# Kernel tuning notes

Hardware: AMD Instinct MI355X
Metric: run time of the kernel (lower is better)

Reference implementation:

```python
import jax, jax.numpy as jnp
import numpy as np

DIM = 256
N_PATCHES = 2048
N_HEADS = 8
BATCH = 2


def setup_inputs() -> dict:
    key = jax.random.key(0)
    ks = jax.random.split(key, 8)
    d = DIM
    s = d ** -0.5
    return {
        "x": jax.random.normal(ks[0], (BATCH, N_PATCHES, d), dtype=jnp.float32),
        # weights stored (in_features, out_features) so y = x @ W + b
        "W_qk": jax.random.normal(ks[1], (d, 2 * d), dtype=jnp.float32) * s,
        "W_v": jax.random.normal(ks[2], (d, d), dtype=jnp.float32) * s,
        "W_proj": jax.random.normal(ks[3], (d, d), dtype=jnp.float32) * s,
        "b_proj": jnp.zeros((d,), dtype=jnp.float32),
        "W_pos": jax.random.normal(ks[4], (2, N_HEADS), dtype=jnp.float32) * 0.5,
        "b_pos": jnp.zeros((N_HEADS,), dtype=jnp.float32),
        "gating": jnp.ones((N_HEADS,), dtype=jnp.float32),
    }


def reference(x, W_qk, W_v, W_proj, b_proj, W_pos, b_pos, gating):
    B, N, C = x.shape
    H = gating.shape[0]
    Dh = C // H
    scale = Dh ** -0.5

    # content attention: q @ k^T softmax
    qk = (x @ W_qk).reshape(B, N, 2, H, Dh)
    q = jnp.transpose(qk[:, :, 0], (0, 2, 1, 3))  # [B,H,N,Dh]
    k = jnp.transpose(qk[:, :, 1], (0, 2, 1, 3))
    patch_score = jax.nn.softmax(jnp.einsum("bhnd,bhmd->bhnm", q, k) * scale, axis=-1)

    # positional attention from relative indices (d, |d|) -> per-head score
    idx = jnp.arange(N, dtype=jnp.float32)
    rel = idx[:, None] - idx[None, :]                      # [N,N]
    rel_feat = jnp.stack([rel, jnp.abs(rel)], axis=-1)     # [N,N,2]
    pos = rel_feat @ W_pos + b_pos                         # [N,N,H]
    pos_score = jax.nn.softmax(jnp.transpose(pos, (2, 0, 1)), axis=-1)  # [H,N,N]

    g = jax.nn.sigmoid(gating)[None, :, None, None]        # [1,H,1,1]
    attn = (1.0 - g) * patch_score + g * pos_score[None]   # [B,H,N,N]
    attn = attn / jnp.sum(attn, axis=-1, keepdims=True)

    v = jnp.transpose((x @ W_v).reshape(B, N, H, Dh), (0, 2, 1, 3))  # [B,H,N,Dh]
    out = jnp.einsum("bhnm,bhmd->bhnd", attn, v)
    out = jnp.transpose(out, (0, 2, 1, 3)).reshape(B, N, C)
    return out @ W_proj + b_proj
```

## Files before the change

kernel.cpp:

```cpp
#include <hip/hip_runtime.h>
#include <hip/hip_bf16.h>

#define DIM 256
#define NP 2048
#define NH 8
#define BATCH 2
#define DH 32

typedef __attribute__((ext_vector_type(8))) short bshort8;
typedef __attribute__((ext_vector_type(4))) short bshort4;
typedef __attribute__((ext_vector_type(4))) float f32x4;

#define LOG2E 1.44269504f
#define QSCALE (0.17677669529663687f * LOG2E)

union U16B { uint4 u; bshort8 s8; __hip_bfloat16 h[8]; };
union U8B  { uint2 u; bshort4 s4; __hip_bfloat16 h[4]; };

__device__ __forceinline__ float fexp2(float x) { return __builtin_amdgcn_exp2f(x); }
__device__ __forceinline__ unsigned packbf(float hi, float lo) {
    return __builtin_amdgcn_perm(__float_as_uint(hi), __float_as_uint(lo), 0x07060302u);
}

__global__ __launch_bounds__(256) void prep_kernel(
    const float* __restrict__ x,
    const float* __restrict__ Wqk,
    const float* __restrict__ Wv,
    const float* __restrict__ Wproj,
    __hip_bfloat16* __restrict__ WT,
    __hip_bfloat16* __restrict__ xb) {
    const int t = threadIdx.x;
    const int blk = blockIdx.x;
    if (blk < 64) {
        __shared__ float ts[64][65];
        const int ct = blk >> 2, k0 = (blk & 3) * 64;
        const int c0 = ct * 64;
        const float* src; int ldw, cs0; float scl = 1.0f;
        if (ct < 8)       { src = Wqk;   ldw = 512; cs0 = c0;      if (ct < 4) scl = QSCALE; }
        else if (ct < 12) { src = Wv;    ldw = 256; cs0 = c0 - 512; }
        else              { src = Wproj; ldw = 256; cs0 = c0 - 768; }
        const int cc = t & 63, tq = t >> 6;
#pragma unroll
        for (int j = 0; j < 16; j++) {
            int kk = tq * 16 + j;
            ts[kk][cc] = src[(size_t)(k0 + kk) * ldw + cs0 + cc];
        }
        __syncthreads();
        const int kk2 = t & 63;
#pragma unroll
        for (int j = 0; j < 16; j++) {
            int cc2 = tq * 16 + j;
            WT[(size_t)(c0 + cc2) * 256 + k0 + kk2] = __float2bfloat16(ts[kk2][cc2] * scl);
        }
    } else {
        const size_t i0 = (size_t)(blk - 64) * 2048 + (size_t)t * 8;
        float4 f0 = *(const float4*)(x + i0);
        float4 f1 = *(const float4*)(x + i0 + 4);
        U16B o;
        o.h[0] = __float2bfloat16(f0.x); o.h[1] = __float2bfloat16(f0.y);
        o.h[2] = __float2bfloat16(f0.z); o.h[3] = __float2bfloat16(f0.w);
        o.h[4] = __float2bfloat16(f1.x); o.h[5] = __float2bfloat16(f1.y);
        o.h[6] = __float2bfloat16(f1.z); o.h[7] = __float2bfloat16(f1.w);
        *(uint4*)(xb + i0) = o.u;
    }
}

__global__ __launch_bounds__(256) void qkv_mfma(
    const __hip_bfloat16* __restrict__ xb,
    const __hip_bfloat16* __restrict__ WT,
    __hip_bfloat16* __restrict__ q,
    __hip_bfloat16* __restrict__ k,
    __hip_bfloat16* __restrict__ vT) {
    const int t = threadIdx.x, lane = t & 63, wvid = t >> 6;
    const int l15 = lane & 15, l4 = lane >> 4;
    const int m0 = blockIdx.x * 64;
    const int nbase = blockIdx.y * 64 + wvid * 16;
    const int nc = nbase + l15;

    f32x4 acc[4] = {{0.f,0.f,0.f,0.f},{0.f,0.f,0.f,0.f},{0.f,0.f,0.f,0.f},{0.f,0.f,0.f,0.f}};
    const __hip_bfloat16* brow = WT + (size_t)nc * 256 + l4 * 8;
    const __hip_bfloat16* arow = xb + (size_t)(m0 + l15) * 256 + l4 * 8;

#pragma unroll
    for (int k0 = 0; k0 < 256; k0 += 32) {
        U16B bw; bw.u = *(const uint4*)(brow + k0);
#pragma unroll
        for (int mt = 0; mt < 4; mt++) {
            U16B ax; ax.u = *(const uint4*)(arow + (size_t)mt * 16 * 256 + k0);
            acc[mt] = __builtin_amdgcn_mfma_f32_16x16x32_bf16(ax.s8, bw.s8, acc[mt], 0, 0, 0);
        }
    }

    if (nbase < 256) {
        const int h = nc >> 5, d = nc & 31;
#pragma unroll
        for (int mt = 0; mt < 4; mt++)
#pragma unroll
            for (int r = 0; r < 4; r++) {
                int tok = m0 + mt * 16 + l4 * 4 + r;
                int b = tok >> 11, n = tok & (NP - 1);
                q[((size_t)(b * NH + h) * NP + n) * DH + d] = __float2bfloat16(acc[mt][r]);
            }
    } else if (nbase < 512) {
        const int c = nc - 256, h = c >> 5, d = c & 31;
#pragma unroll
        for (int mt = 0; mt < 4; mt++)
#pragma unroll
            for (int r = 0; r < 4; r++) {
                int tok = m0 + mt * 16 + l4 * 4 + r;
                int b = tok >> 11, n = tok & (NP - 1);
                k[((size_t)(b * NH + h) * NP + n) * DH + d] = __float2bfloat16(acc[mt][r]);
            }
    } else {
        const int c = nc - 512;
        const int b = m0 >> 11;
#pragma unroll
        for (int mt = 0; mt < 4; mt++) {
            int tokn = (m0 & (NP - 1)) + mt * 16 + l4 * 4;
            U8B vv;
#pragma unroll
            for (int r = 0; r < 4; r++) vv.h[r] = __float2bfloat16(acc[mt][r]);
            *(uint2*)(vT + (size_t)(b * 256 + c) * NP + tokn) = vv.u;
        }
    }
}

__global__ __launch_bounds__(512, 4) void attn_kernel(
    const __hip_bfloat16* __restrict__ qg,
    const __hip_bfloat16* __restrict__ kg,
    const __hip_bfloat16* __restrict__ vTg,
    const float* __restrict__ Wpos,
    const float* __restrict__ bpos,
    const float* __restrict__ gating,
    __hip_bfloat16* __restrict__ ao) {
    __shared__ __align__(16) __hip_bfloat16 Kt[2][2][64][40];
    __shared__ __align__(16) __hip_bfloat16 Vt[2][2][32][68];
    __shared__ float cmb[4][2][32][16];
    __shared__ float cls[4][2][16];

    const int t = threadIdx.x;
    const int lane = t & 63, wvid = t >> 6;
    const int l15 = lane & 15, l4 = lane >> 4;
    const int qt = wvid & 3, kh = wvid >> 2;
    const int bh = blockIdx.x >> 5, qb = blockIdx.x & 31;
    const int h = bh & (NH - 1), b = bh >> 3;
    const int q0 = qb * 64 + qt * 16;
    const int myq = q0 + l15;

    const int st_ = t & 255;
    const int kstart = kh * 1024;
    const __hip_bfloat16* kptr = kg + (size_t)bh * NP * DH + (size_t)(kstart + (st_ >> 2)) * DH + (st_ & 3) * 8;
    const __hip_bfloat16* vptr = vTg + ((size_t)bh * DH + (st_ >> 3)) * NP + kstart + (st_ & 7) * 8;

    uint4 kreg = *(const uint4*)kptr;
    uint4 vreg = *(const uint4*)vptr;
    *(uint4*)&Kt[kh][0][st_ >> 2][(st_ & 3) * 8] = kreg;
    *(uint2*)&Vt[kh][0][st_ >> 3][(st_ & 7) * 8]     = make_uint2(vreg.x, vreg.y);
    *(uint2*)&Vt[kh][0][st_ >> 3][(st_ & 7) * 8 + 4] = make_uint2(vreg.z, vreg.w);

    const float w0 = Wpos[h] * LOG2E;
    const float w1 = Wpos[NH + h] * LOG2E;
    const float g = 1.0f / (1.0f + __expf(-gating[h]));
    const float nf = (float)myq;
    const float pmax = fmaxf(0.f, fmaxf((w0 + w1) * nf, (w1 - w0) * (2047.0f - nf)));
    const float npmax = -pmax;
    const float rA = fexp2(-(w0 + w1));
    const float rB = fexp2(w1 - w0);

    U16B qv;
    qv.u = *(const uint4*)(qg + ((size_t)bh * NP + myq) * DH + l4 * 8);

    __syncthreads();

    f32x4 os0 = {0.f,0.f,0.f,0.f}, os1 = {0.f,0.f,0.f,0.f};
    f32x4 op0 = {0.f,0.f,0.f,0.f}, op1 = {0.f,0.f,0.f,0.f};
    float ls = 0.f, lp = 0.f;

    for (int it = 0; it < 16; ++it) {
        const int cur = it & 1, nxt = cur ^ 1;

        if (it < 15) {
            kreg = *(const uint4*)(kptr + (size_t)(it + 1) * 64 * DH);
            vreg = *(const uint4*)(vptr + (it + 1) * 64);
        }

        f32x4 st4[4];
#pragma unroll
        for (int kt = 0; kt < 4; kt++) {
            U16B kf; kf.u = *(const uint4*)&Kt[kh][cur][kt * 16 + l15][l4 * 8];
            st4[kt] = __builtin_amdgcn_mfma_f32_16x16x32_bf16(
                kf.s8, qv.s8, (f32x4){0.f,0.f,0.f,0.f}, 0, 0, 0);
        }

        U8B vfr[8];
#pragma unroll
        for (int vh = 0; vh < 2; vh++)
#pragma unroll
            for (int kt = 0; kt < 4; kt++)
                vfr[vh * 4 + kt].u = *(const uint2*)&Vt[kh][cur][vh * 16 + l15][kt * 16 + l4 * 4];

        const int kb0 = kstart + it * 64;
#pragma unroll
        for (int kt = 0; kt < 4; kt++) {
            float es0 = fexp2(st4[kt][0]), es1 = fexp2(st4[kt][1]);
            float es2 = fexp2(st4[kt][2]), es3 = fexp2(st4[kt][3]);
            ls += (es0 + es1) + (es2 + es3);
            const float d0 = nf - (float)(kb0 + kt * 16 + l4 * 4);
            float ep0 = fexp2(fmaf(w1, fabsf(d0), fmaf(w0, d0, npmax)));
            float ep1 = ep0 * ((d0 >= 1.f) ? rA : rB);
            float ep2 = ep1 * ((d0 >= 2.f) ? rA : rB);
            float ep3 = ep2 * ((d0 >= 3.f) ? rA : rB);
            lp += (ep0 + ep1) + (ep2 + ep3);
            U8B pc, pp;
            pc.u.x = packbf(es1, es0); pc.u.y = packbf(es3, es2);
            pp.u.x = packbf(ep1, ep0); pp.u.y = packbf(ep3, ep2);
            os0 = __builtin_amdgcn_mfma_f32_16x16x16bf16_1k(vfr[kt].s4,     pc.s4, os0, 0, 0, 0);
            os1 = __builtin_amdgcn_mfma_f32_16x16x16bf16_1k(vfr[4 + kt].s4, pc.s4, os1, 0, 0, 0);
            op0 = __builtin_amdgcn_mfma_f32_16x16x16bf16_1k(vfr[kt].s4,     pp.s4, op0, 0, 0, 0);
            op1 = __builtin_amdgcn_mfma_f32_16x16x16bf16_1k(vfr[4 + kt].s4, pp.s4, op1, 0, 0, 0);
        }

        if (it < 15) {
            *(uint4*)&Kt[kh][nxt][st_ >> 2][(st_ & 3) * 8] = kreg;
            *(uint2*)&Vt[kh][nxt][st_ >> 3][(st_ & 7) * 8]     = make_uint2(vreg.x, vreg.y);
            *(uint2*)&Vt[kh][nxt][st_ >> 3][(st_ & 7) * 8 + 4] = make_uint2(vreg.z, vreg.w);
        }
        __syncthreads();
    }

    ls += __shfl_xor(ls, 16, 64); ls += __shfl_xor(ls, 32, 64);
    lp += __shfl_xor(lp, 16, 64); lp += __shfl_xor(lp, 32, 64);

    if (kh == 1) {
#pragma unroll
        for (int r = 0; r < 4; r++) {
            cmb[qt][0][l4 * 4 + r][l15]      = os0[r];
            cmb[qt][0][16 + l4 * 4 + r][l15] = os1[r];
            cmb[qt][1][l4 * 4 + r][l15]      = op0[r];
            cmb[qt][1][16 + l4 * 4 + r][l15] = op1[r];
        }
        if (l4 == 0) { cls[qt][0][l15] = ls; cls[qt][1][l15] = lp; }
    }
    __syncthreads();
    if (kh == 0) {
        ls += cls[qt][0][l15]; lp += cls[qt][1][l15];
        const float cs = (1.0f - g) / ls;
        const float cp = g / lp;
        const size_t orow = ((size_t)b * NP + myq) * DIM + h * DH;
        U8B o0, o1;
#pragma unroll
        for (int r = 0; r < 4; r++) {
            o0.h[r] = __float2bfloat16(cs * (os0[r] + cmb[qt][0][l4 * 4 + r][l15]) +
                                       cp * (op0[r] + cmb[qt][1][l4 * 4 + r][l15]));
            o1.h[r] = __float2bfloat16(cs * (os1[r] + cmb[qt][0][16 + l4 * 4 + r][l15]) +
                                       cp * (op1[r] + cmb[qt][1][16 + l4 * 4 + r][l15]));
        }
        *(uint2*)(ao + orow + l4 * 4)      = o0.u;
        *(uint2*)(ao + orow + 16 + l4 * 4) = o1.u;
    }
}

__global__ __launch_bounds__(256) void proj_mfma(
    const __hip_bfloat16* __restrict__ ao,
    const __hip_bfloat16* __restrict__ WT,
    const float* __restrict__ bias,
    float* __restrict__ out) {
    const int t = threadIdx.x, lane = t & 63, wvid = t >> 6;
    const int l15 = lane & 15, l4 = lane >> 4;
    const int m0 = blockIdx.x * 64;
    const int nc = blockIdx.y * 64 + wvid * 16 + l15;

    f32x4 acc[4] = {{0.f,0.f,0.f,0.f},{0.f,0.f,0.f,0.f},{0.f,0.f,0.f,0.f},{0.f,0.f,0.f,0.f}};
    const __hip_bfloat16* brow = WT + (size_t)(768 + nc) * 256 + l4 * 8;
    const __hip_bfloat16* arow = ao + (size_t)(m0 + l15) * 256 + l4 * 8;

#pragma unroll
    for (int k0 = 0; k0 < 256; k0 += 32) {
        U16B bw; bw.u = *(const uint4*)(brow + k0);
#pragma unroll
        for (int mt = 0; mt < 4; mt++) {
            U16B ax; ax.u = *(const uint4*)(arow + (size_t)mt * 16 * 256 + k0);
            acc[mt] = __builtin_amdgcn_mfma_f32_16x16x32_bf16(ax.s8, bw.s8, acc[mt], 0, 0, 0);
        }
    }

    const float bb = bias[nc];
#pragma unroll
    for (int mt = 0; mt < 4; mt++)
#pragma unroll
        for (int r = 0; r < 4; r++) {
            int tok = m0 + mt * 16 + l4 * 4 + r;
            out[(size_t)tok * 256 + nc] = acc[mt][r] + bb;
        }
}

extern "C" void kernel_launch(void* const* d_in, const int* in_sizes, int n_in,
                              void* d_out, int out_size, void* d_ws, size_t ws_size,
                              hipStream_t stream) {
    const float* x      = (const float*)d_in[0];
    const float* Wqk    = (const float*)d_in[1];
    const float* Wv     = (const float*)d_in[2];
    const float* Wproj  = (const float*)d_in[3];
    const float* bproj  = (const float*)d_in[4];
    const float* Wpos   = (const float*)d_in[5];
    const float* bpos   = (const float*)d_in[6];
    const float* gating = (const float*)d_in[7];
    float* out = (float*)d_out;

    const size_t nElem = (size_t)BATCH * NP * DIM;
    char* w = (char*)d_ws;
    __hip_bfloat16* xb = (__hip_bfloat16*)w;
    __hip_bfloat16* ao = xb;
    __hip_bfloat16* WT = xb + nElem;
    __hip_bfloat16* q  = WT + 262144;
    __hip_bfloat16* k  = q + nElem;
    __hip_bfloat16* vT = k + nElem;

    prep_kernel<<<576, 256, 0, stream>>>(x, Wqk, Wv, Wproj, WT, xb);
    qkv_mfma<<<dim3(64, 12), 256, 0, stream>>>(xb, WT, q, k, vT);
    attn_kernel<<<BATCH * NH * (NP / 64), 512, 0, stream>>>(q, k, vT, Wpos, bpos, gating, ao);
    proj_mfma<<<dim3(64, 4), 256, 0, stream>>>(ao, WT, bproj, out);
}
```

Before: 119.6 us.

## Fuse x bf16 conversion into QKV GEMM and stage GEMM tiles in swizzled LDS

The x-to-bf16 conversion moves out of the prep kernel and into the QKV GEMM, which now reads fp32 x directly, converts it, and stores it in a swizzled LDS tile. Both the QKV and projection GEMMs now stage full 64x256 A and B tiles in XOR-swizzled shared memory with coalesced loads, instead of each wave reading fragments straight from global memory. This drops one workspace round-trip for xb and shrinks the prep launch to the weight transpose only. In exchange, each QKV block redundantly converts its x tile across all 12 column blocks, and the 64 KB of LDS per block limits occupancy.

```diff
diff --git a/kernel.cpp b/kernel.cpp
--- a/kernel.cpp
+++ b/kernel.cpp
@@ -22,76 +22,82 @@
     return __builtin_amdgcn_perm(__float_as_uint(hi), __float_as_uint(lo), 0x07060302u);
 }
 
+__device__ __forceinline__ int lds_addr(int row, int colg) {
+    return row * 256 + (((colg ^ (row & 7)) & 31) << 3);
+}
+
 __global__ __launch_bounds__(256) void prep_kernel(
-    const float* __restrict__ x,
     const float* __restrict__ Wqk,
     const float* __restrict__ Wv,
     const float* __restrict__ Wproj,
-    __hip_bfloat16* __restrict__ WT,
-    __hip_bfloat16* __restrict__ xb) {
+    __hip_bfloat16* __restrict__ WT) {
     const int t = threadIdx.x;
     const int blk = blockIdx.x;
-    if (blk < 64) {
-        __shared__ float ts[64][65];
-        const int ct = blk >> 2, k0 = (blk & 3) * 64;
-        const int c0 = ct * 64;
-        const float* src; int ldw, cs0; float scl = 1.0f;
-        if (ct < 8)       { src = Wqk;   ldw = 512; cs0 = c0;      if (ct < 4) scl = QSCALE; }
-        else if (ct < 12) { src = Wv;    ldw = 256; cs0 = c0 - 512; }
-        else              { src = Wproj; ldw = 256; cs0 = c0 - 768; }
-        const int cc = t & 63, tq = t >> 6;
-#pragma unroll
-        for (int j = 0; j < 16; j++) {
-            int kk = tq * 16 + j;
-            ts[kk][cc] = src[(size_t)(k0 + kk) * ldw + cs0 + cc];
-        }
-        __syncthreads();
-        const int kk2 = t & 63;
-#pragma unroll
-        for (int j = 0; j < 16; j++) {
-            int cc2 = tq * 16 + j;
-            WT[(size_t)(c0 + cc2) * 256 + k0 + kk2] = __float2bfloat16(ts[kk2][cc2] * scl);
-        }
-    } else {
-        const size_t i0 = (size_t)(blk - 64) * 2048 + (size_t)t * 8;
-        float4 f0 = *(const float4*)(x + i0);
-        float4 f1 = *(const float4*)(x + i0 + 4);
-        U16B o;
-        o.h[0] = __float2bfloat16(f0.x); o.h[1] = __float2bfloat16(f0.y);
-        o.h[2] = __float2bfloat16(f0.z); o.h[3] = __float2bfloat16(f0.w);
-        o.h[4] = __float2bfloat16(f1.x); o.h[5] = __float2bfloat16(f1.y);
-        o.h[6] = __float2bfloat16(f1.z); o.h[7] = __float2bfloat16(f1.w);
-        *(uint4*)(xb + i0) = o.u;
+    __shared__ float ts[64][65];
+    const int ct = blk >> 2, k0 = (blk & 3) * 64;
+    const int c0 = ct * 64;
+    const float* src; int ldw, cs0; float scl = 1.0f;
+    if (ct < 8)       { src = Wqk;   ldw = 512; cs0 = c0;      if (ct < 4) scl = QSCALE; }
+    else if (ct < 12) { src = Wv;    ldw = 256; cs0 = c0 - 512; }
+    else              { src = Wproj; ldw = 256; cs0 = c0 - 768; }
+    const int cc = t & 63, tq = t >> 6;
+#pragma unroll
+    for (int j = 0; j < 16; j++) {
+        int kk = tq * 16 + j;
+        ts[kk][cc] = src[(size_t)(k0 + kk) * ldw + cs0 + cc];
+    }
+    __syncthreads();
+    const int kk2 = t & 63;
+#pragma unroll
+    for (int j = 0; j < 16; j++) {
+        int cc2 = tq * 16 + j;
+        WT[(size_t)(c0 + cc2) * 256 + k0 + kk2] = __float2bfloat16(ts[kk2][cc2] * scl);
     }
 }
 
 __global__ __launch_bounds__(256) void qkv_mfma(
-    const __hip_bfloat16* __restrict__ xb,
+    const float* __restrict__ x,
     const __hip_bfloat16* __restrict__ WT,
     __hip_bfloat16* __restrict__ q,
     __hip_bfloat16* __restrict__ k,
     __hip_bfloat16* __restrict__ vT) {
+    __shared__ __align__(16) __hip_bfloat16 As[64 * 256];
+    __shared__ __align__(16) __hip_bfloat16 Bs[64 * 256];
     const int t = threadIdx.x, lane = t & 63, wvid = t >> 6;
     const int l15 = lane & 15, l4 = lane >> 4;
     const int m0 = blockIdx.x * 64;
-    const int nbase = blockIdx.y * 64 + wvid * 16;
-    const int nc = nbase + l15;
+    const int nb0 = blockIdx.y * 64;
+    const int nc = nb0 + wvid * 16 + l15;
+
+#pragma unroll
+    for (int j = 0; j < 8; j++) {
+        const int flat = j * 2048 + t * 8;
+        const int row = flat >> 8, colg = (flat >> 3) & 31;
+        float4 f0 = *(const float4*)(x + (size_t)m0 * 256 + flat);
+        float4 f1 = *(const float4*)(x + (size_t)m0 * 256 + flat + 4);
+        U16B a;
+        a.h[0] = __float2bfloat16(f0.x); a.h[1] = __float2bfloat16(f0.y);
+        a.h[2] = __float2bfloat16(f0.z); a.h[3] = __float2bfloat16(f0.w);
+        a.h[4] = __float2bfloat16(f1.x); a.h[5] = __float2bfloat16(f1.y);
+        a.h[6] = __float2bfloat16(f1.z); a.h[7] = __float2bfloat16(f1.w);
+        *(uint4*)&As[lds_addr(row, colg)] = a.u;
+        *(uint4*)&Bs[lds_addr(row, colg)] = *(const uint4*)(WT + (size_t)nb0 * 256 + flat);
+    }
+    __syncthreads();
 
     f32x4 acc[4] = {{0.f,0.f,0.f,0.f},{0.f,0.f,0.f,0.f},{0.f,0.f,0.f,0.f},{0.f,0.f,0.f,0.f}};
-    const __hip_bfloat16* brow = WT + (size_t)nc * 256 + l4 * 8;
-    const __hip_bfloat16* arow = xb + (size_t)(m0 + l15) * 256 + l4 * 8;
-
-#pragma unroll
-    for (int k0 = 0; k0 < 256; k0 += 32) {
-        U16B bw; bw.u = *(const uint4*)(brow + k0);
+#pragma unroll
+    for (int kk = 0; kk < 8; kk++) {
+        const int colg = kk * 4 + l4;
+        U16B bw; bw.u = *(const uint4*)&Bs[lds_addr(wvid * 16 + l15, colg)];
 #pragma unroll
         for (int mt = 0; mt < 4; mt++) {
-            U16B ax; ax.u = *(const uint4*)(arow + (size_t)mt * 16 * 256 + k0);
+            U16B ax; ax.u = *(const uint4*)&As[lds_addr(mt * 16 + l15, colg)];
             acc[mt] = __builtin_amdgcn_mfma_f32_16x16x32_bf16(ax.s8, bw.s8, acc[mt], 0, 0, 0);
         }
     }
 
-    if (nbase < 256) {
+    if (nb0 < 256) {
         const int h = nc >> 5, d = nc & 31;
 #pragma unroll
         for (int mt = 0; mt < 4; mt++)
@@ -101,7 +107,7 @@
                 int b = tok >> 11, n = tok & (NP - 1);
                 q[((size_t)(b * NH + h) * NP + n) * DH + d] = __float2bfloat16(acc[mt][r]);
             }
-    } else if (nbase < 512) {
+    } else if (nb0 < 512) {
         const int c = nc - 256, h = c >> 5, d = c & 31;
 #pragma unroll
         for (int mt = 0; mt < 4; mt++)
@@ -265,21 +271,31 @@
     const __hip_bfloat16* __restrict__ WT,
     const float* __restrict__ bias,
     float* __restrict__ out) {
+    __shared__ __align__(16) __hip_bfloat16 As[64 * 256];
+    __shared__ __align__(16) __hip_bfloat16 Bs[64 * 256];
     const int t = threadIdx.x, lane = t & 63, wvid = t >> 6;
     const int l15 = lane & 15, l4 = lane >> 4;
     const int m0 = blockIdx.x * 64;
-    const int nc = blockIdx.y * 64 + wvid * 16 + l15;
+    const int nb0 = blockIdx.y * 64;
+    const int nc = nb0 + wvid * 16 + l15;
+
+#pragma unroll
+    for (int j = 0; j < 8; j++) {
+        const int flat = j * 2048 + t * 8;
+        const int row = flat >> 8, colg = (flat >> 3) & 31;
+        *(uint4*)&As[lds_addr(row, colg)] = *(const uint4*)(ao + (size_t)m0 * 256 + flat);
+        *(uint4*)&Bs[lds_addr(row, colg)] = *(const uint4*)(WT + (size_t)(768 + nb0) * 256 + flat);
+    }
+    __syncthreads();
 
     f32x4 acc[4] = {{0.f,0.f,0.f,0.f},{0.f,0.f,0.f,0.f},{0.f,0.f,0.f,0.f},{0.f,0.f,0.f,0.f}};
-    const __hip_bfloat16* brow = WT + (size_t)(768 + nc) * 256 + l4 * 8;
-    const __hip_bfloat16* arow = ao + (size_t)(m0 + l15) * 256 + l4 * 8;
-
-#pragma unroll
-    for (int k0 = 0; k0 < 256; k0 += 32) {
-        U16B bw; bw.u = *(const uint4*)(brow + k0);
+#pragma unroll
+    for (int kk = 0; kk < 8; kk++) {
+        const int colg = kk * 4 + l4;
+        U16B bw; bw.u = *(const uint4*)&Bs[lds_addr(wvid * 16 + l15, colg)];
 #pragma unroll
         for (int mt = 0; mt < 4; mt++) {
-            U16B ax; ax.u = *(const uint4*)(arow + (size_t)mt * 16 * 256 + k0);
+            U16B ax; ax.u = *(const uint4*)&As[lds_addr(mt * 16 + l15, colg)];
             acc[mt] = __builtin_amdgcn_mfma_f32_16x16x32_bf16(ax.s8, bw.s8, acc[mt], 0, 0, 0);
         }
     }
@@ -309,15 +325,14 @@
 
     const size_t nElem = (size_t)BATCH * NP * DIM;
     char* w = (char*)d_ws;
-    __hip_bfloat16* xb = (__hip_bfloat16*)w;
-    __hip_bfloat16* ao = xb;
-    __hip_bfloat16* WT = xb + nElem;
+    __hip_bfloat16* WT = (__hip_bfloat16*)w;
     __hip_bfloat16* q  = WT + 262144;
     __hip_bfloat16* k  = q + nElem;
     __hip_bfloat16* vT = k + nElem;
-
-    prep_kernel<<<576, 256, 0, stream>>>(x, Wqk, Wv, Wproj, WT, xb);
-    qkv_mfma<<<dim3(64, 12), 256, 0, stream>>>(xb, WT, q, k, vT);
+    __hip_bfloat16* ao = vT + nElem;
+
+    prep_kernel<<<64, 256, 0, stream>>>(Wqk, Wv, Wproj, WT);
+    qkv_mfma<<<dim3(64, 12), 256, 0, stream>>>(x, WT, q, k, vT);
     attn_kernel<<<BATCH * NH * (NP / 64), 512, 0, stream>>>(q, k, vT, Wpos, bpos, gating, ao);
     proj_mfma<<<dim3(64, 4), 256, 0, stream>>>(ao, WT, bproj, out);
 }
```

Measured after the change: 107.4 us. 1.11x faster.
